# Kernel optimization log

Measured on AMD Instinct MI355X. Metric: run time of the kernel, lower is better.

The kernel has to match this reference:

```python
import jax, jax.numpy as jnp
import numpy as np

B, S, D, FD = 2, 2048, 1024, 4096
EPS_LN = 1e-5


def _l2norm(x):
    n = jnp.linalg.norm(x, axis=-1, keepdims=True)
    return x / jnp.maximum(n, 1e-12)


def _layernorm(x, w, b):
    m = x.mean(-1, keepdims=True)
    v = ((x - m) ** 2).mean(-1, keepdims=True)
    return (x - m) / jnp.sqrt(v + EPS_LN) * w + b


def _spl(x, mu_w, mu_b, gate, proto):
    # cosine-similarity gated linear (SparseProtoLinear)
    scores = _l2norm(x) @ _l2norm(proto).T          # [..., out]
    rw = jax.nn.relu(scores - gate)
    comp = x @ mu_w.T + mu_b
    return comp * rw


def _rotate_half(x):
    h = x.shape[-1] // 2
    return jnp.concatenate([-x[..., h:], x[..., :h]], axis=-1)


def _forward(x, cos, sin,
             ln1_w, ln1_b, ln2_w, ln2_b,
             qkv_mu, qkv_proto, qkv_bias, qkv_gate,
             o_mu, o_proto, o_bias, o_gate,
             f1_mu, f1_proto, f1_bias, f1_gate,
             f2_mu, f2_proto, f2_bias, f2_gate,
             pt_qkv, pt_o, pt_f1, pt_f2,
             pln_qkv_w, pln_qkv_b, pln_o_w, pln_o_b,
             pln_f1_w, pln_f1_b, pln_f2_w, pln_f2_b,
             prev_qkv, prev_o, prev_f1, prev_f2):
    # effective protos: proto_weight + LN(Linear(prev_proto))
    eff_qkv = qkv_proto + _layernorm(prev_qkv @ pt_qkv.T, pln_qkv_w, pln_qkv_b)
    eff_o   = o_proto   + _layernorm(prev_o   @ pt_o.T,   pln_o_w,   pln_o_b)
    eff_f1  = f1_proto  + _layernorm(prev_f1  @ pt_f1.T,  pln_f1_w,  pln_f1_b)
    eff_f2  = f2_proto  + _layernorm(prev_f2  @ pt_f2.T,  pln_f2_w,  pln_f2_b)

    # attention
    attn_in = _layernorm(x, ln1_w, ln1_b)
    m_qkv = _spl(attn_in, qkv_mu, qkv_bias, qkv_gate, eff_qkv)   # [B,S,3D]
    q, k, v = jnp.split(m_qkv, 3, axis=-1)
    c = cos[None]; s = sin[None]
    q = q * c + _rotate_half(q) * s
    k = k * c + _rotate_half(k) * s
    scale = 1.0 / jnp.sqrt(jnp.asarray(D, x.dtype))
    scores = jnp.einsum('bqd,bkd->bqk', q, k) * scale            # [B,S,S]
    causal = jnp.tril(jnp.ones((S, S), dtype=bool))
    scores = jnp.where(causal[None], scores, jnp.finfo(x.dtype).min)
    attn = jax.nn.softmax(scores, axis=-1)
    attn_out = jnp.einsum('bqk,bkd->bqd', attn, v)
    m_o = _spl(attn_out, o_mu, o_bias, o_gate, eff_o)
    x1 = x + m_o

    # ffn (DynamicInfiniteExpert)
    ffn_in = _layernorm(x1, ln2_w, ln2_b)
    m1 = _spl(ffn_in, f1_mu, f1_bias, f1_gate, eff_f1)           # [B,S,FD]
    h = jax.nn.relu(m1)
    m2 = _spl(h, f2_mu, f2_bias, f2_gate, eff_f2)                # [B,S,D]
    return x1 + m2


def setup_inputs() -> dict:
    key = jax.random.key(0)
    ks = iter(jax.random.split(key, 64))

    def nrm(shape, scale=1.0):
        return jax.random.normal(next(ks), shape, dtype=jnp.float32) * scale

    # RoPE tables
    pos = np.arange(S, dtype=np.float32)
    inv_freq = 1.0 / (10000.0 ** (np.arange(0, D, 2, dtype=np.float32) / D))
    freqs = np.outer(pos, inv_freq)
    emb = np.concatenate([freqs, freqs], axis=-1)
    cos = jnp.asarray(np.cos(emb)); sin = jnp.asarray(np.sin(emb))

    sD = 1.0 / np.sqrt(D); sF = 1.0 / np.sqrt(FD)
    inp = {
        'x': nrm((B, S, D)), 'cos': cos, 'sin': sin,
        'ln1_w': jnp.ones((D,)), 'ln1_b': jnp.zeros((D,)),
        'ln2_w': jnp.ones((D,)), 'ln2_b': jnp.zeros((D,)),
        'qkv_mu': nrm((3 * D, D), sD), 'qkv_proto': nrm((3 * D, D), sD),
        'qkv_bias': jnp.zeros((3 * D,)), 'qkv_gate': jnp.zeros((3 * D,)),
        'o_mu': nrm((D, D), sD), 'o_proto': nrm((D, D), sD),
        'o_bias': jnp.zeros((D,)), 'o_gate': jnp.zeros((D,)),
        'f1_mu': nrm((FD, D), sD), 'f1_proto': nrm((FD, D), sD),
        'f1_bias': jnp.zeros((FD,)), 'f1_gate': jnp.zeros((FD,)),
        'f2_mu': nrm((D, FD), sF), 'f2_proto': nrm((D, FD), sF),
        'f2_bias': jnp.zeros((D,)), 'f2_gate': jnp.zeros((D,)),
        'pt_qkv': nrm((D, D), sD), 'pt_o': nrm((D, D), sD),
        'pt_f1': nrm((D, D), sD), 'pt_f2': nrm((FD, FD), sF),
        'pln_qkv_w': jnp.ones((D,)), 'pln_qkv_b': jnp.zeros((D,)),
        'pln_o_w': jnp.ones((D,)), 'pln_o_b': jnp.zeros((D,)),
        'pln_f1_w': jnp.ones((D,)), 'pln_f1_b': jnp.zeros((D,)),
        'pln_f2_w': jnp.ones((FD,)), 'pln_f2_b': jnp.zeros((FD,)),
        'prev_qkv': nrm((3 * D, D), sD), 'prev_o': nrm((D, D), sD),
        'prev_f1': nrm((FD, D), sD), 'prev_f2': nrm((D, FD), sF),
    }
    return inp


def reference(x, cos, sin,
              ln1_w, ln1_b, ln2_w, ln2_b,
              qkv_mu, qkv_proto, qkv_bias, qkv_gate,
              o_mu, o_proto, o_bias, o_gate,
              f1_mu, f1_proto, f1_bias, f1_gate,
              f2_mu, f2_proto, f2_bias, f2_gate,
              pt_qkv, pt_o, pt_f1, pt_f2,
              pln_qkv_w, pln_qkv_b, pln_o_w, pln_o_b,
              pln_f1_w, pln_f1_b, pln_f2_w, pln_f2_b,
              prev_qkv, prev_o, prev_f1, prev_f2):
    return _forward(x, cos, sin, ln1_w, ln1_b, ln2_w, ln2_b,
                    qkv_mu, qkv_proto, qkv_bias, qkv_gate,
                    o_mu, o_proto, o_bias, o_gate,
                    f1_mu, f1_proto, f1_bias, f1_gate,
                    f2_mu, f2_proto, f2_bias, f2_gate,
                    pt_qkv, pt_o, pt_f1, pt_f2,
                    pln_qkv_w, pln_qkv_b, pln_o_w, pln_o_b,
                    pln_f1_w, pln_f1_b, pln_f2_w, pln_f2_b,
                    prev_qkv, prev_o, prev_f1, prev_f2)
```

## Files before the change

### kernel.cpp

```cpp
#include <hip/hip_runtime.h>
#include <cstdint>

typedef unsigned short u16;
typedef __attribute__((ext_vector_type(8))) short sh8;
typedef __attribute__((ext_vector_type(4))) float f32x4;

struct __align__(8) us4 { u16 x, y, z, w; };

__device__ __forceinline__ u16 f2bf(float f) {
  unsigned u = __float_as_uint(f);
  u += 0x7FFFu + ((u >> 16) & 1u);
  return (u16)(u >> 16);
}
__device__ __forceinline__ float bf2f(u16 h) {
  return __uint_as_float((unsigned)h << 16);
}
__device__ __forceinline__ float invnorm(float nrm) {
  return fminf(rsqrtf(nrm), 1e12f);
}

__device__ __forceinline__ float blk_sum(float v, float* red) {
#pragma unroll
  for (int o = 32; o; o >>= 1) v += __shfl_xor(v, o);
  __syncthreads();
  if ((threadIdx.x & 63) == 0) red[threadIdx.x >> 6] = v;
  __syncthreads();
  return red[0] + red[1] + red[2] + red[3];
}
__device__ __forceinline__ float blk_max(float v, float* red) {
#pragma unroll
  for (int o = 32; o; o >>= 1) v = fmaxf(v, __shfl_xor(v, o));
  __syncthreads();
  if ((threadIdx.x & 63) == 0) red[threadIdx.x >> 6] = v;
  __syncthreads();
  return fmaxf(fmaxf(red[0], red[1]), fmaxf(red[2], red[3]));
}

__global__ void fillv(float* __restrict__ o, long n, float v) {
  long i = (long)blockIdx.x * blockDim.x + threadIdx.x;
  if (i < n) o[i] = v;
}

struct CvtN10 {
  const float* s[10];
  u16* d[10];
  long n4[10];
};
__global__ void cvt_many(CvtN10 c) {
  int z = blockIdx.y;
  long i = (long)blockIdx.x * blockDim.x + threadIdx.x;
  if (i >= c.n4[z]) return;
  float4 v = ((const float4*)c.s[z])[i];
  us4 o; o.x = f2bf(v.x); o.y = f2bf(v.y); o.z = f2bf(v.z); o.w = f2bf(v.w);
  ((us4*)c.d[z])[i] = o;
}

#define GL16(gp, lp)                                                        \
  __builtin_amdgcn_global_load_lds(                                         \
      (const __attribute__((address_space(1))) void*)(gp),                  \
      (__attribute__((address_space(3))) void*)(lp), 16, 0, 0)

#define G256_PROLOG()                                                          \
  extern __shared__ u16 lds[];                                                 \
  int tid = threadIdx.x;                                                       \
  int wid = tid >> 6, lane = tid & 63;                                         \
  int wm = wid >> 2, wn = wid & 3;                                             \
  int bm = blockIdx.x, bn = blockIdx.y;                                        \
  int k0s = 0, nt;                                                             \
  if (kchunk) {                                                                \
    k0s = blockIdx.z * kchunk;                                                 \
    nt = kchunk >> 5;                                                          \
  } else {                                                                     \
    nt = K >> 5;                                                               \
  }                                                                            \
  const size_t baseArow = (size_t)bm * 256;                                    \
  const size_t baseBrow = (size_t)bn * 256;                                    \
  int ci = (wid << 6) + lane;                                                  \
  int rowS = ci >> 2;                                                          \
  int kcS = (ci ^ (ci >> 3)) & 3;                                              \
  const u16* gA0 = A + (baseArow + rowS) * lda + k0s + kcS * 8;                \
  const u16* gA1 = gA0 + (size_t)128 * lda;                                    \
  const u16* gB0 = B + (baseBrow + rowS) * ldb + k0s + kcS * 8;                \
  const u16* gB1 = gB0 + (size_t)128 * ldb;                                    \
  u16* dBase = lds + (wid << 9);                                               \
  int l15 = lane & 15, l4 = lane >> 4;                                         \
  int aoff[8], boff[4];                                                        \
  _Pragma("unroll") for (int fr = 0; fr < 8; ++fr) {                           \
    int by = (wm * 128 + fr * 16 + l15) * 64 + l4 * 16;                        \
    aoff[fr] = (by ^ (((by >> 7) & 3) << 4)) >> 1;                             \
  }                                                                            \
  _Pragma("unroll") for (int fc = 0; fc < 4; ++fc) {                           \
    int by = (wn * 64 + fc * 16 + l15) * 64 + l4 * 16;                         \
    boff[fc] = 8192 + ((by ^ (((by >> 7) & 3) << 4)) >> 1);                    \
  }                                                                            \
  f32x4 acc[8][4];                                                             \
  const f32x4 zf = {0.f, 0.f, 0.f, 0.f};                                       \
  _Pragma("unroll") for (int i = 0; i < 8; ++i)                                \
    _Pragma("unroll") for (int j = 0; j < 4; ++j) acc[i][j] = zf;

#define STAGE256(ts)                                                  \
  do {                                                                \
    int ss_ = (ts) & 3;                                               \
    int kk_ = (ts) << 5;                                              \
    u16* d_ = dBase + ss_ * 16384;                                    \
    GL16(gA0 + kk_, d_);                                              \
    GL16(gA1 + kk_, d_ + 4096);                                       \
    GL16(gB0 + kk_, d_ + 8192);                                       \
    GL16(gB1 + kk_, d_ + 12288);                                      \
  } while (0)

#define G256_KLOOP()                                                           \
  STAGE256(0);                                                                 \
  STAGE256(1);                                                                 \
  STAGE256(2);                                                                 \
  asm volatile("s_waitcnt vmcnt(8)" ::: "memory");                             \
  __builtin_amdgcn_s_barrier();                                                \
  __builtin_amdgcn_sched_barrier(0);                                           \
  for (int t = 0; t < nt; ++t) {                                               \
    int ts = t + 3;                                                            \
    if (ts < nt) STAGE256(ts);                                                 \
    const u16* sl = lds + (t & 3) * 16384;                                     \
    sh8 af[8], bfv[4];                                                         \
    _Pragma("unroll") for (int fc = 0; fc < 4; ++fc)                           \
        bfv[fc] = *(const sh8*)(sl + boff[fc]);                                \
    _Pragma("unroll") for (int fr = 0; fr < 8; ++fr)                           \
        af[fr] = *(const sh8*)(sl + aoff[fr]);                                 \
    __builtin_amdgcn_s_setprio(1);                                             \
    _Pragma("unroll") for (int fr = 0; fr < 8; ++fr)                           \
      _Pragma("unroll") for (int fc = 0; fc < 4; ++fc)                         \
        acc[fr][fc] = __builtin_amdgcn_mfma_f32_16x16x32_bf16(                 \
            af[fr], bfv[fc], acc[fr][fc], 0, 0, 0);                            \
    __builtin_amdgcn_s_setprio(0);                                             \
    int rem = nt - 2 - t;                                                      \
    if (rem >= 2)      asm volatile("s_waitcnt vmcnt(8)" ::: "memory");        \
    else if (rem == 1) asm volatile("s_waitcnt vmcnt(4)" ::: "memory");        \
    else if (rem == 0) asm volatile("s_waitcnt vmcnt(0)" ::: "memory");        \
    if (t < nt - 1) {                                                          \
      __builtin_amdgcn_s_barrier();                                            \
      __builtin_amdgcn_sched_barrier(0);                                       \
    }                                                                          \
  }

template <typename CT>
__global__ __launch_bounds__(512, 1) void gemm256(
    const u16* __restrict__ A, const u16* __restrict__ B, CT* __restrict__ C,
    int M, int N, int K, int lda, int ldb, int kchunk) {
  if (kchunk) C += (size_t)blockIdx.z * M * (size_t)N;
  G256_PROLOG();
  G256_KLOOP();
  int cr = l4 << 2, cc = l15;
  const size_t rbase = baseArow + wm * 128 + cr;
  const size_t cbase = baseBrow + wn * 64 + cc;
#pragma unroll
  for (int fr = 0; fr < 8; ++fr)
#pragma unroll
    for (int fc = 0; fc < 4; ++fc) {
      size_t cb = (rbase + fr * 16) * (size_t)N + cbase + fc * 16;
#pragma unroll
      for (int r = 0; r < 4; ++r) {
        float v = acc[fr][fc][r];
        if constexpr (sizeof(CT) == 2) C[cb + (size_t)r * N] = (CT)f2bf(v);
        else                           C[cb + (size_t)r * N] = v;
      }
    }
}

template <typename CT>
__global__ __launch_bounds__(256, 2) void gemm_bt(
    const u16* __restrict__ A, const u16* __restrict__ B, CT* __restrict__ C,
    int M, int N, int K, int lda, int ldb,
    int mode, long zsA, long zsB, long zsC) {
  int bm, bn;
  int z = blockIdx.z;
  if (mode == 3) {
    int t = blockIdx.x;
    int m = (int)floorf((sqrtf(8.f * t + 1.f) - 1.f) * 0.5f);
    while ((m + 1) * (m + 2) / 2 <= t) ++m;
    while (m * (m + 1) / 2 > t) --m;
    bm = m; bn = t - m * (m + 1) / 2;
  } else {
    bm = blockIdx.x; bn = blockIdx.y;
  }
  int k0s = 0, k0e = K;
  if (mode == 1) {
    int kc = K / gridDim.z;
    k0s = z * kc; k0e = k0s + kc;
    C += (size_t)z * M * (size_t)N;
  } else if (mode == 2 || mode == 3) {
    A += (size_t)z * zsA; B += (size_t)z * zsB; C += (size_t)z * zsC;
  } else if (mode == 4) {
    A += (size_t)z * zsA; B += (size_t)z * zsB; C += (size_t)z * zsC;
    k0e = (bm + 1) * 128;
  } else if (mode == 5) {
    int Mz = (int)((zsB >> (z * 16)) & 0xFFFF);
    if (bm * 128 >= Mz) return;
    A += (size_t)z * zsA; B += (size_t)z * 1048576; C += (size_t)z * zsC;
  }

  __shared__ __align__(16) u16 As[128 * 32];
  __shared__ __align__(16) u16 Bs[128 * 32];
  int tid = threadIdx.x, wid = tid >> 6, lane = tid & 63;
  int wr = (wid >> 1) << 6, wc = (wid & 1) << 6;
  int lr = lane & 15, lk = (lane >> 4) << 3;

  f32x4 acc[4][4];
  const f32x4 zf = {0.f, 0.f, 0.f, 0.f};
#pragma unroll
  for (int i = 0; i < 4; ++i)
#pragma unroll
    for (int j = 0; j < 4; ++j) acc[i][j] = zf;

  int r0 = tid >> 2, c0 = (tid & 3) << 3;
  const size_t baseA = (size_t)bm * 128, baseB = (size_t)bn * 128;
  const u16* Ab = A + baseA * lda;
  const u16* Bp = B + baseB * ldb;

  for (int k0 = k0s; k0 < k0e; k0 += 32) {
    GL16(Ab + (size_t)r0 * lda + k0 + c0, As + (wid << 9));
    GL16(Ab + (size_t)(64 + r0) * lda + k0 + c0, As + 2048 + (wid << 9));
    GL16(Bp + (size_t)r0 * ldb + k0 + c0, Bs + (wid << 9));
    GL16(Bp + (size_t)(64 + r0) * ldb + k0 + c0, Bs + 2048 + (wid << 9));
    __syncthreads();
    sh8 af[4], bfr[4];
#pragma unroll
    for (int f = 0; f < 4; ++f) {
      af[f]  = *(const sh8*)(As + (wr + f * 16 + lr) * 32 + lk);
      bfr[f] = *(const sh8*)(Bs + (wc + f * 16 + lr) * 32 + lk);
    }
#pragma unroll
    for (int i = 0; i < 4; ++i)
#pragma unroll
      for (int j = 0; j < 4; ++j)
        acc[i][j] = __builtin_amdgcn_mfma_f32_16x16x32_bf16(af[i], bfr[j], acc[i][j], 0, 0, 0);
    __syncthreads();
  }

  int cr = (lane >> 4) << 2, cc = lane & 15;
#pragma unroll
  for (int i = 0; i < 4; ++i)
#pragma unroll
    for (int j = 0; j < 4; ++j) {
      size_t cb = (baseA + wr + i * 16 + cr) * (size_t)N + (baseB + wc + j * 16 + cc);
#pragma unroll
      for (int r = 0; r < 4; ++r) {
        float v = acc[i][j][r];
        if constexpr (sizeof(CT) == 2) C[cb + (size_t)r * N] = (CT)f2bf(v);
        else                           C[cb + (size_t)r * N] = v;
      }
    }
}

__global__ void ln_rows(const float* __restrict__ X, const float* __restrict__ w,
                        const float* __restrict__ b, u16* __restrict__ Y,
                        float* __restrict__ norms, int C) {
  __shared__ float red[4];
  int row = blockIdx.x;
  const float* x = X + (size_t)row * C;
  int nv = C >> 2;
  float s = 0.f, ss = 0.f;
  for (int i = threadIdx.x; i < nv; i += 256) {
    float4 v = ((const float4*)x)[i];
    s += v.x + v.y + v.z + v.w;
    ss += v.x * v.x + v.y * v.y + v.z * v.z + v.w * v.w;
  }
  s = blk_sum(s, red);
  ss = blk_sum(ss, red);
  float mean = s / C;
  float inv = rsqrtf(fmaxf(ss / C - mean * mean, 0.f) + 1e-5f);
  float nrm = 0.f;
  for (int i = threadIdx.x; i < nv; i += 256) {
    float4 v = ((const float4*)x)[i];
    float4 wv = ((const float4*)w)[i];
    float4 bv = ((const float4*)b)[i];
    float y0 = (v.x - mean) * inv * wv.x + bv.x;
    float y1 = (v.y - mean) * inv * wv.y + bv.y;
    float y2 = (v.z - mean) * inv * wv.z + bv.z;
    float y3 = (v.w - mean) * inv * wv.w + bv.w;
    nrm += y0 * y0 + y1 * y1 + y2 * y2 + y3 * y3;
    us4 o; o.x = f2bf(y0); o.y = f2bf(y1); o.z = f2bf(y2); o.w = f2bf(y3);
    ((us4*)(Y + (size_t)row * C))[i] = o;
  }
  nrm = blk_sum(nrm, red);
  if (threadIdx.x == 0) norms[row] = invnorm(nrm);
}

__global__ void ln_add_norm(const u16* __restrict__ T0, const u16* __restrict__ T1,
                            const float* __restrict__ P,
                            const float* __restrict__ w, const float* __restrict__ b,
                            u16* __restrict__ E, float* __restrict__ norms, int C) {
  __shared__ float red[4];
  int row = blockIdx.x;
  const us4* t0 = (const us4*)(T0 + (size_t)row * C);
  const us4* t1 = T1 ? (const us4*)(T1 + (size_t)row * C) : nullptr;
  const float* p = P + (size_t)row * C;
  int nv = C >> 2;
  float s = 0.f, ss = 0.f;
  for (int i = threadIdx.x; i < nv; i += 256) {
    us4 v = t0[i];
    float f0 = bf2f(v.x), f1 = bf2f(v.y), f2 = bf2f(v.z), f3 = bf2f(v.w);
    if (t1) {
      us4 v1 = t1[i];
      f0 += bf2f(v1.x); f1 += bf2f(v1.y); f2 += bf2f(v1.z); f3 += bf2f(v1.w);
    }
    s += f0 + f1 + f2 + f3;
    ss += f0 * f0 + f1 * f1 + f2 * f2 + f3 * f3;
  }
  s = blk_sum(s, red);
  ss = blk_sum(ss, red);
  float mean = s / C;
  float inv = rsqrtf(fmaxf(ss / C - mean * mean, 0.f) + 1e-5f);
  float nrm = 0.f;
  for (int i = threadIdx.x; i < nv; i += 256) {
    us4 v = t0[i];
    float f0 = bf2f(v.x), f1 = bf2f(v.y), f2 = bf2f(v.z), f3 = bf2f(v.w);
    if (t1) {
      us4 v1 = t1[i];
      f0 += bf2f(v1.x); f1 += bf2f(v1.y); f2 += bf2f(v1.z); f3 += bf2f(v1.w);
    }
    float4 pv = ((const float4*)p)[i];
    float4 wv = ((const float4*)w)[i];
    float4 bv = ((const float4*)b)[i];
    float y0 = pv.x + (f0 - mean) * inv * wv.x + bv.x;
    float y1 = pv.y + (f1 - mean) * inv * wv.y + bv.y;
    float y2 = pv.z + (f2 - mean) * inv * wv.z + bv.z;
    float y3 = pv.w + (f3 - mean) * inv * wv.w + bv.w;
    nrm += y0 * y0 + y1 * y1 + y2 * y2 + y3 * y3;
    us4 o; o.x = f2bf(y0); o.y = f2bf(y1); o.z = f2bf(y2); o.w = f2bf(y3);
    *(us4*)(E + (size_t)row * C + (i << 2)) = o;
  }
  nrm = blk_sum(nrm, red);
  if (threadIdx.x == 0) norms[row] = invnorm(nrm);
}

struct Lan3 {
  const u16* T[3];
  const float* P[3]; const float* w[3]; const float* b[3];
  u16* E[3]; float* nr[3]; int M[3];
};
__global__ void lan_many(Lan3 L) {
  __shared__ float red[4];
  int z = blockIdx.y;
  int row = blockIdx.x;
  if (row >= L.M[z]) return;
  int i = threadIdx.x;
  us4 v = ((const us4*)(L.T[z] + (size_t)row * 1024))[i];
  float f0 = bf2f(v.x), f1 = bf2f(v.y), f2 = bf2f(v.z), f3 = bf2f(v.w);
  float s = blk_sum(f0 + f1 + f2 + f3, red);
  float ss = blk_sum(f0 * f0 + f1 * f1 + f2 * f2 + f3 * f3, red);
  float mean = s * (1.f / 1024.f);
  float inv = rsqrtf(fmaxf(ss * (1.f / 1024.f) - mean * mean, 0.f) + 1e-5f);
  float4 pv = ((const float4*)(L.P[z] + (size_t)row * 1024))[i];
  float4 wv = ((const float4*)L.w[z])[i];
  float4 bv = ((const float4*)L.b[z])[i];
  float y0 = pv.x + (f0 - mean) * inv * wv.x + bv.x;
  float y1 = pv.y + (f1 - mean) * inv * wv.y + bv.y;
  float y2 = pv.z + (f2 - mean) * inv * wv.z + bv.z;
  float y3 = pv.w + (f3 - mean) * inv * wv.w + bv.w;
  us4 o; o.x = f2bf(y0); o.y = f2bf(y1); o.z = f2bf(y2); o.w = f2bf(y3);
  ((us4*)(L.E[z] + (size_t)row * 1024))[i] = o;
  float nrm = blk_sum(y0 * y0 + y1 * y1 + y2 * y2 + y3 * y3, red);
  if (threadIdx.x == 0) L.nr[z][row] = invnorm(nrm);
}

__global__ void rownorm_bf(const u16* __restrict__ X, float* __restrict__ norms, int C) {
  __shared__ float red[4];
  int row = blockIdx.x;
  const us4* x = (const us4*)(X + (size_t)row * C);
  int nv = C >> 2;
  float nrm = 0.f;
  for (int i = threadIdx.x; i < nv; i += 256) {
    us4 v = x[i];
    float a = bf2f(v.x), b = bf2f(v.y), c = bf2f(v.z), d = bf2f(v.w);
    nrm += a * a + b * b + c * c + d * d;
  }
  nrm = blk_sum(nrm, red);
  if (threadIdx.x == 0) norms[row] = invnorm(nrm);
}

__device__ __forceinline__ void epi4(const u16* gr, int C, int c, float rr,
                                     const float* bias, const float* gate,
                                     const float* cn, float* o) {
  us4 cv = *(const us4*)(gr + c);
  us4 dv = *(const us4*)(gr + C + c);
  float4 bv = *(const float4*)(bias + c);
  float4 gv = *(const float4*)(gate + c);
  float4 nv = *(const float4*)(cn + c);
  float cf[4] = {bf2f(cv.x), bf2f(cv.y), bf2f(cv.z), bf2f(cv.w)};
  float df[4] = {bf2f(dv.x), bf2f(dv.y), bf2f(dv.z), bf2f(dv.w)};
  float bb[4] = {bv.x, bv.y, bv.z, bv.w};
  float gg[4] = {gv.x, gv.y, gv.z, gv.w};
  float nn[4] = {nv.x, nv.y, nv.z, nv.w};
#pragma unroll
  for (int j = 0; j < 4; ++j) {
    float sc = df[j] * (rr * nn[j]);
    o[j] = (cf[j] + bb[j]) * fmaxf(sc - gg[j], 0.f);
  }
}

__global__ void spl_rope_row(const u16* __restrict__ G, const float* __restrict__ bias,
                             const float* __restrict__ gate, const float* __restrict__ rn,
                             const float* __restrict__ cn, const float* __restrict__ CT_,
                             const float* __restrict__ ST_, u16* __restrict__ MQ) {
  int r = blockIdx.x;
  int s = r & 2047;
  const u16* gr = G + (size_t)r * 6144;
  u16* outr = MQ + (size_t)r * 3072;
  float rr = rn[r];
  int t = threadIdx.x;

  int qk = (t >> 7);
  int c = qk * 1024 + ((t & 127) << 2);
  int d = c - qk * 1024;
  float a0[4], a1[4];
  epi4(gr, 3072, c, rr, bias, gate, cn, a0);
  epi4(gr, 3072, c + 512, rr, bias, gate, cn, a1);
  const float* ct = CT_ + (size_t)s * 1024;
  const float* st = ST_ + (size_t)s * 1024;
  float4 c0 = *(const float4*)(ct + d);
  float4 s0 = *(const float4*)(st + d);
  float4 c1 = *(const float4*)(ct + d + 512);
  float4 s1 = *(const float4*)(st + d + 512);
  float cc0[4] = {c0.x, c0.y, c0.z, c0.w}, ss0[4] = {s0.x, s0.y, s0.z, s0.w};
  float cc1[4] = {c1.x, c1.y, c1.z, c1.w}, ss1[4] = {s1.x, s1.y, s1.z, s1.w};
  us4 o0, o1;
  o0.x = f2bf(a0[0] * cc0[0] - a1[0] * ss0[0]);
  o0.y = f2bf(a0[1] * cc0[1] - a1[1] * ss0[1]);
  o0.z = f2bf(a0[2] * cc0[2] - a1[2] * ss0[2]);
  o0.w = f2bf(a0[3] * cc0[3] - a1[3] * ss0[3]);
  o1.x = f2bf(a1[0] * cc1[0] + a0[0] * ss1[0]);
  o1.y = f2bf(a1[1] * cc1[1] + a0[1] * ss1[1]);
  o1.z = f2bf(a1[2] * cc1[2] + a0[2] * ss1[2]);
  o1.w = f2bf(a1[3] * cc1[3] + a0[3] * ss1[3]);
  *(us4*)(outr + c) = o0;
  *(us4*)(outr + c + 512) = o1;

  int cv_ = 2048 + (t << 2);
  float vv[4];
  epi4(gr, 3072, cv_, rr, bias, gate, cn, vv);
  us4 ov; ov.x = f2bf(vv[0]); ov.y = f2bf(vv[1]); ov.z = f2bf(vv[2]); ov.w = f2bf(vv[3]);
  *(us4*)(outr + cv_) = ov;
}

__global__ void spl_f1_row(const u16* __restrict__ G, const float* __restrict__ bias,
                           const float* __restrict__ gate, const float* __restrict__ rn,
                           const float* __restrict__ cn, u16* __restrict__ H,
                           float* __restrict__ rn_h) {
  __shared__ float red[4];
  int r = blockIdx.x;
  const u16* gr = G + (size_t)r * 8192;
  u16* hr = H + (size_t)r * 4096;
  float rr = rn[r];
  float nrm = 0.f;
  for (int c = threadIdx.x << 2; c < 4096; c += 1024) {
    float o[4];
    epi4(gr, 4096, c, rr, bias, gate, cn, o);
#pragma unroll
    for (int j = 0; j < 4; ++j) {
      o[j] = fmaxf(o[j], 0.f);
      nrm += o[j] * o[j];
    }
    us4 ov; ov.x = f2bf(o[0]); ov.y = f2bf(o[1]); ov.z = f2bf(o[2]); ov.w = f2bf(o[3]);
    *(us4*)(hr + c) = ov;
  }
  nrm = blk_sum(nrm, red);
  if (threadIdx.x == 0) rn_h[r] = invnorm(nrm);
}

__global__ void spl_o_ln_row(const u16* __restrict__ G, const float* __restrict__ bias,
                             const float* __restrict__ gate, const float* __restrict__ rn,
                             const float* __restrict__ cn, const float* __restrict__ xres,
                             const float* __restrict__ lw, const float* __restrict__ lb,
                             float* __restrict__ X1, u16* __restrict__ Y,
                             float* __restrict__ rn_ffn) {
  __shared__ float red[4];
  int r = blockIdx.x;
  int c = threadIdx.x << 2;
  const u16* gr = G + (size_t)r * 2048;
  float o[4];
  epi4(gr, 1024, c, rn[r], bias, gate, cn, o);
  float4 rv = *(const float4*)(xres + (size_t)r * 1024 + c);
  o[0] += rv.x; o[1] += rv.y; o[2] += rv.z; o[3] += rv.w;
  float4 xo = {o[0], o[1], o[2], o[3]};
  *(float4*)(X1 + (size_t)r * 1024 + c) = xo;
  float s = o[0] + o[1] + o[2] + o[3];
  float ss = o[0] * o[0] + o[1] * o[1] + o[2] * o[2] + o[3] * o[3];
  s = blk_sum(s, red);
  ss = blk_sum(ss, red);
  float mean = s * (1.f / 1024.f);
  float inv = rsqrtf(fmaxf(ss * (1.f / 1024.f) - mean * mean, 0.f) + 1e-5f);
  float4 wv = *(const float4*)(lw + c);
  float4 bv = *(const float4*)(lb + c);
  float ww[4] = {wv.x, wv.y, wv.z, wv.w}, bb[4] = {bv.x, bv.y, bv.z, bv.w};
  float nrm = 0.f;
  us4 ov;
  u16* op = (u16*)&ov;
#pragma unroll
  for (int j = 0; j < 4; ++j) {
    float y = (o[j] - mean) * inv * ww[j] + bb[j];
    nrm += y * y;
    op[j] = f2bf(y);
  }
  *(us4*)(Y + (size_t)r * 1024 + c) = ov;
  nrm = blk_sum(nrm, red);
  if (threadIdx.x == 0) rn_ffn[r] = invnorm(nrm);
}

__global__ void spl_epi_p(const u16* __restrict__ G0, const u16* __restrict__ G1,
                          const float* __restrict__ bias, const float* __restrict__ gate,
                          const float* __restrict__ rn, const float* __restrict__ cn,
                          const float* __restrict__ resid, float* __restrict__ out) {
  int r = blockIdx.x;
  int c = threadIdx.x << 2;
  size_t rowb = (size_t)r * 2048;
  us4 c0 = *(const us4*)(G0 + rowb + c);
  us4 c1 = *(const us4*)(G1 + rowb + c);
  us4 d0 = *(const us4*)(G0 + rowb + 1024 + c);
  us4 d1 = *(const us4*)(G1 + rowb + 1024 + c);
  float4 bv = *(const float4*)(bias + c);
  float4 gv = *(const float4*)(gate + c);
  float4 nv = *(const float4*)(cn + c);
  float4 rv = *(const float4*)(resid + (size_t)r * 1024 + c);
  float rr = rn[r];
  float cf[4] = {bf2f(c0.x) + bf2f(c1.x), bf2f(c0.y) + bf2f(c1.y),
                 bf2f(c0.z) + bf2f(c1.z), bf2f(c0.w) + bf2f(c1.w)};
  float df[4] = {bf2f(d0.x) + bf2f(d1.x), bf2f(d0.y) + bf2f(d1.y),
                 bf2f(d0.z) + bf2f(d1.z), bf2f(d0.w) + bf2f(d1.w)};
  float bb[4] = {bv.x, bv.y, bv.z, bv.w};
  float gg[4] = {gv.x, gv.y, gv.z, gv.w};
  float nn[4] = {nv.x, nv.y, nv.z, nv.w};
  float re[4] = {rv.x, rv.y, rv.z, rv.w};
  float4 ov;
  float* op = (float*)&ov;
#pragma unroll
  for (int j = 0; j < 4; ++j) {
    float sc = df[j] * (rr * nn[j]);
    op[j] = (cf[j] + bb[j]) * fmaxf(sc - gg[j], 0.f) + re[j];
  }
  *(float4*)(out + (size_t)r * 1024 + c) = ov;
}

__global__ void vtrans(const u16* __restrict__ MQ, u16* __restrict__ VT) {
  __shared__ u16 tile[32][33];
  int b = blockIdx.z;
  int s0 = blockIdx.x << 5, d0 = blockIdx.y << 5;
  int tx = threadIdx.x, ty = threadIdx.y;
  for (int r = ty; r < 32; r += 8)
    tile[r][tx] = MQ[((size_t)(b * 2048 + s0 + r)) * 3072 + 2048 + d0 + tx];
  __syncthreads();
  for (int r = ty; r < 32; r += 8)
    VT[(size_t)b * 1024 * 2048 + (size_t)(d0 + r) * 2048 + s0 + tx] = tile[tx][r];
}

__global__ void softmax_causal(const float* __restrict__ S, u16* __restrict__ P) {
  __shared__ float red[4];
  int b = blockIdx.x >> 11;
  int q = blockIdx.x & 2047;
  const float* row = S + ((size_t)b << 22) + (size_t)q * 2048;
  u16* prow = P + ((size_t)b << 22) + (size_t)q * 2048;
  int nv = q + 1;
  int wcap = ((q >> 7) + 1) << 7;
  int base = threadIdx.x * 8;
  float e[8];
  float m = -3.4e38f;
  float xv[8];
  bool live = base < nv;
  if (live) {
    float4 a = *(const float4*)(row + base);
    float4 bq = *(const float4*)(row + base + 4);
    xv[0] = a.x; xv[1] = a.y; xv[2] = a.z; xv[3] = a.w;
    xv[4] = bq.x; xv[5] = bq.y; xv[6] = bq.z; xv[7] = bq.w;
#pragma unroll
    for (int j = 0; j < 8; ++j) {
      xv[j] *= 0.03125f;
      if (base + j < nv) m = fmaxf(m, xv[j]);
    }
  }
  m = blk_max(m, red);
  float ssum = 0.f;
#pragma unroll
  for (int j = 0; j < 8; ++j) {
    e[j] = (live && base + j < nv) ? __expf(xv[j] - m) : 0.f;
    ssum += e[j];
  }
  ssum = blk_sum(ssum, red);
  float invs = 1.f / ssum;
  if (base < wcap) {
    us4 o;
    o.x = f2bf(e[0] * invs); o.y = f2bf(e[1] * invs);
    o.z = f2bf(e[2] * invs); o.w = f2bf(e[3] * invs);
    ((us4*)prow)[threadIdx.x * 2] = o;
    o.x = f2bf(e[4] * invs); o.y = f2bf(e[5] * invs);
    o.z = f2bf(e[6] * invs); o.w = f2bf(e[7] * invs);
    ((us4*)prow)[threadIdx.x * 2 + 1] = o;
  }
}

extern "C" void kernel_launch(void* const* d_in, const int* in_sizes, int n_in,
                              void* d_out, int out_size, void* d_ws, size_t ws_size,
                              hipStream_t stream) {
  (void)in_sizes;
  const float* x         = (const float*)d_in[0];
  const float* cosT      = (const float*)d_in[1];
  const float* sinT      = (const float*)d_in[2];
  const float* ln1_w     = (const float*)d_in[3];
  const float* ln1_b     = (const float*)d_in[4];
  const float* ln2_w     = (const float*)d_in[5];
  const float* ln2_b     = (const float*)d_in[6];
  const float* qkv_mu    = (const float*)d_in[7];
  const float* qkv_proto = (const float*)d_in[8];
  const float* qkv_bias  = (const float*)d_in[9];
  const float* qkv_gate  = (const float*)d_in[10];
  const float* o_mu      = (const float*)d_in[11];
  const float* o_proto   = (const float*)d_in[12];
  const float* o_bias    = (const float*)d_in[13];
  const float* o_gate    = (const float*)d_in[14];
  const float* f1_mu     = (const float*)d_in[15];
  const float* f1_proto  = (const float*)d_in[16];
  const float* f1_bias   = (const float*)d_in[17];
  const float* f1_gate   = (const float*)d_in[18];
  const float* f2_mu     = (const float*)d_in[19];
  const float* f2_proto  = (const float*)d_in[20];
  const float* f2_bias   = (const float*)d_in[21];
  const float* f2_gate   = (const float*)d_in[22];
  const float* pt_qkv    = (const float*)d_in[23];
  const float* pt_o      = (const float*)d_in[24];
  const float* pt_f1     = (const float*)d_in[25];
  const float* pt_f2     = (const float*)d_in[26];
  const float* pln_qkv_w = (const float*)d_in[27];
  const float* pln_qkv_b = (const float*)d_in[28];
  const float* pln_o_w   = (const float*)d_in[29];
  const float* pln_o_b   = (const float*)d_in[30];
  const float* pln_f1_w  = (const float*)d_in[31];
  const float* pln_f1_b  = (const float*)d_in[32];
  const float* pln_f2_w  = (const float*)d_in[33];
  const float* pln_f2_b  = (const float*)d_in[34];
  const float* prev_qkv  = (const float*)d_in[35];
  const float* prev_o    = (const float*)d_in[36];
  const float* prev_f1   = (const float*)d_in[37];
  const float* prev_f2   = (const float*)d_in[38];

  const long D = 1024, TD = 3072, FD = 4096, R = 4096;

  char* W = (char*)d_ws;
  size_t off = 0;
  auto alloc = [&](size_t bytes) {
    void* p = W + off;
    off = (off + bytes + 255) & ~(size_t)255;
    return p;
  };
  char* GOUT = (char*)alloc(67108864);
  u16*  RC   = (u16*)alloc(33554432);
  u16*  wq   = (u16*)alloc(2 * TD * D * 2);
  u16*  wo   = (u16*)alloc(2 * D * D * 2);
  u16*  wf1  = (u16*)alloc(2 * FD * D * 2);
  u16*  wf2  = (u16*)alloc(2 * D * FD * 2);
  float* X1  = (float*)alloc(R * D * 4);
  u16*  P1   = (u16*)alloc(R * D * 2);
  u16*  VT   = (u16*)alloc(2 * D * 2048 * 2);
  u16*  AOB  = (u16*)alloc(R * D * 2);
  float* pnq     = (float*)alloc(TD * 4);
  float* pno     = (float*)alloc(D * 4);
  float* pnf1    = (float*)alloc(FD * 4);
  float* pnf2    = (float*)alloc(D * 4);
  float* rn_ain  = (float*)alloc(R * 4);
  float* rn_aout = (float*)alloc(R * 4);
  float* rn_ffn  = (float*)alloc(R * 4);
  float* rn_h    = (float*)alloc(R * 4);
  size_t need = off;

  if (n_in < 39 || need > ws_size) {
    long n = out_size;
    fillv<<<dim3((unsigned)((n + 255) / 256)), 256, 0, stream>>>((float*)d_out, n, 12345.0f);
    return;
  }

  u16* SA = (u16*)GOUT;
  u16* SB = (u16*)(GOUT + 25165824);
  float* SCORES = (float*)GOUT;
  u16* PB = (u16*)(GOUT + 33554432);

  {
    CvtN10 c;
    c.s[0] = prev_f1;  c.d[0] = SA;            c.n4[0] = (FD * D) >> 2;
    c.s[1] = prev_qkv; c.d[1] = SA + 4194304;  c.n4[1] = (TD * D) >> 2;
    c.s[2] = prev_o;   c.d[2] = SA + 8388608;  c.n4[2] = (D * D) >> 2;
    c.s[3] = pt_f1;    c.d[3] = SB;            c.n4[3] = (D * D) >> 2;
    c.s[4] = pt_qkv;   c.d[4] = SB + 1048576;  c.n4[4] = (D * D) >> 2;
    c.s[5] = pt_o;     c.d[5] = SB + 2097152;  c.n4[5] = (D * D) >> 2;
    c.s[6] = qkv_mu;   c.d[6] = wq;            c.n4[6] = (TD * D) >> 2;
    c.s[7] = f1_mu;    c.d[7] = wf1;           c.n4[7] = (FD * D) >> 2;
    c.s[8] = o_mu;     c.d[8] = wo;            c.n4[8] = (D * D) >> 2;
    c.s[9] = f2_mu;    c.d[9] = wf2;           c.n4[9] = (D * FD) >> 2;
    cvt_many<<<dim3(4096, 10), 256, 0, stream>>>(c);
  }
  {
    long Mz = 4096L | (3072L << 16) | (1024L << 32);
    gemm_bt<u16><<<dim3(32, 8, 3), 256, 0, stream>>>(
        SA, SB, RC, 4096, 1024, 1024, 1024, 1024, 5, 4194304, Mz, 4194304);
  }
  {
    Lan3 L;
    L.T[0] = RC;           L.P[0] = f1_proto;  L.w[0] = pln_f1_w;  L.b[0] = pln_f1_b;
    L.E[0] = wf1 + (size_t)FD * D;  L.nr[0] = pnf1;  L.M[0] = 4096;
    L.T[1] = RC + 4194304; L.P[1] = qkv_proto; L.w[1] = pln_qkv_w; L.b[1] = pln_qkv_b;
    L.E[1] = wq + (size_t)TD * D;   L.nr[1] = pnq;   L.M[1] = 3072;
    L.T[2] = RC + 8388608; L.P[2] = o_proto;   L.w[2] = pln_o_w;   L.b[2] = pln_o_b;
    L.E[2] = wo + (size_t)D * D;    L.nr[2] = pno;   L.M[2] = 1024;
    lan_many<<<dim3(4096, 3), 256, 0, stream>>>(L);
  }
  {
    CvtN10 c = {};
    c.s[0] = prev_f2; c.d[0] = SA; c.n4[0] = (D * FD) >> 2;
    c.s[1] = pt_f2;   c.d[1] = SB; c.n4[1] = ((long)FD * FD) >> 2;
    cvt_many<<<dim3(16384, 2), 256, 0, stream>>>(c);
  }
  gemm_bt<u16><<<dim3(8, 32, 2), 256, 0, stream>>>(
      SA, SB, RC, 1024, 4096, 4096, 4096, 4096, 1, 0, 0, 0);
  ln_add_norm<<<1024, 256, 0, stream>>>(RC, RC + 4194304, f2_proto, pln_f2_w, pln_f2_b,
                                        wf2 + (size_t)D * FD, pnf2, 4096);

  ln_rows<<<4096, 256, 0, stream>>>(x, ln1_w, ln1_b, P1, rn_ain, 1024);
  gemm256<u16><<<dim3(16, 24), 512, 131072, stream>>>(
      P1, wq, (u16*)GOUT, 4096, 6144, 1024, 1024, 1024, 0);
  spl_rope_row<<<4096, 256, 0, stream>>>(
      (u16*)GOUT, qkv_bias, qkv_gate, rn_ain, pnq, cosT, sinT, RC);

  vtrans<<<dim3(64, 32, 2), dim3(32, 8), 0, stream>>>(RC, VT);
  gemm_bt<float><<<dim3(136, 1, 2), 256, 0, stream>>>(
      RC, RC + 1024, SCORES, 2048, 2048, 1024, 3072, 3072,
      3, 2048L * 3072, 2048L * 3072, 1L << 22);
  softmax_causal<<<4096, 256, 0, stream>>>(SCORES, PB);
  gemm_bt<u16><<<dim3(16, 8, 2), 256, 0, stream>>>(
      PB, VT, AOB, 2048, 1024, 2048, 2048, 2048,
      4, 1L << 22, 1024L * 2048, 2048L * 1024);
  rownorm_bf<<<4096, 256, 0, stream>>>(AOB, rn_aout, 1024);

  gemm_bt<u16><<<dim3(32, 16, 1), 256, 0, stream>>>(
      AOB, wo, (u16*)GOUT, 4096, 2048, 1024, 1024, 1024, 0, 0, 0, 0);
  spl_o_ln_row<<<4096, 256, 0, stream>>>(
      (u16*)GOUT, o_bias, o_gate, rn_aout, pno, x, ln2_w, ln2_b, X1, P1, rn_ffn);

  gemm256<u16><<<dim3(16, 32), 512, 131072, stream>>>(
      P1, wf1, (u16*)GOUT, 4096, 8192, 1024, 1024, 1024, 0);
  spl_f1_row<<<4096, 256, 0, stream>>>(
      (u16*)GOUT, f1_bias, f1_gate, rn_ffn, pnf1, RC, rn_h);
  gemm256<u16><<<dim3(16, 8, 2), 512, 131072, stream>>>(
      RC, wf2, (u16*)GOUT, 4096, 2048, 4096, 4096, 4096, 2048);
  spl_epi_p<<<4096, 256, 0, stream>>>(
      (u16*)GOUT, (u16*)GOUT + 8388608, f2_bias, f2_gate, rn_h, pnf2,
      X1, (float*)d_out);
}
```

Before: 558.3 us.

## Add XCD-aware block swizzle, store attention scores in bf16, retile QKV GEMM

Adds an XCD-aware remapping of workgroup indices in both GEMM kernels so that neighbouring tiles land on the same chiplet and share L2. The QK^T scores are now written as bf16 instead of fp32, which halves score-matrix traffic into the softmax. The QKV projection also moves from the 256-tile gemm256 kernel to the 128-tile gemm_bt kernel. Rounding scores to bf16 before the softmax loses some precision, and the smaller tiles for QKV may lower data reuse.

```diff
diff --git a/kernel.cpp b/kernel.cpp
--- a/kernel.cpp
+++ b/kernel.cpp
@@ -17,6 +17,11 @@
 }
 __device__ __forceinline__ float invnorm(float nrm) {
   return fminf(rsqrtf(nrm), 1e12f);
+}
+__device__ __forceinline__ int xcd_swz(int flat, int nwg) {
+  if (nwg & 7) return flat;
+  int q = nwg >> 3;
+  return (flat & 7) * q + (flat >> 3);
 }
 
 __device__ __forceinline__ float blk_sum(float v, float* red) {
@@ -65,7 +70,9 @@
   int tid = threadIdx.x;                                                       \
   int wid = tid >> 6, lane = tid & 63;                                         \
   int wm = wid >> 2, wn = wid & 3;                                             \
-  int bm = blockIdx.x, bn = blockIdx.y;                                        \
+  int flatb = xcd_swz(blockIdx.x + blockIdx.y * gridDim.x,                     \
+                      gridDim.x * gridDim.y);                                  \
+  int bm = flatb % gridDim.x, bn = flatb / gridDim.x;                          \
   int k0s = 0, nt;                                                             \
   if (kchunk) {                                                                \
     k0s = blockIdx.z * kchunk;                                                 \
@@ -173,13 +180,15 @@
   int bm, bn;
   int z = blockIdx.z;
   if (mode == 3) {
-    int t = blockIdx.x;
+    int t = xcd_swz(blockIdx.x, gridDim.x);
     int m = (int)floorf((sqrtf(8.f * t + 1.f) - 1.f) * 0.5f);
     while ((m + 1) * (m + 2) / 2 <= t) ++m;
     while (m * (m + 1) / 2 > t) --m;
     bm = m; bn = t - m * (m + 1) / 2;
   } else {
-    bm = blockIdx.x; bn = blockIdx.y;
+    int flatb = xcd_swz(blockIdx.x + blockIdx.y * gridDim.x,
+                        gridDim.x * gridDim.y);
+    bm = flatb % gridDim.x; bn = flatb / gridDim.x;
   }
   int k0s = 0, k0e = K;
   if (mode == 1) {
@@ -551,11 +560,11 @@
     VT[(size_t)b * 1024 * 2048 + (size_t)(d0 + r) * 2048 + s0 + tx] = tile[tx][r];
 }
 
-__global__ void softmax_causal(const float* __restrict__ S, u16* __restrict__ P) {
+__global__ void softmax_causal(const u16* __restrict__ S, u16* __restrict__ P) {
   __shared__ float red[4];
   int b = blockIdx.x >> 11;
   int q = blockIdx.x & 2047;
-  const float* row = S + ((size_t)b << 22) + (size_t)q * 2048;
+  const u16* row = S + ((size_t)b << 22) + (size_t)q * 2048;
   u16* prow = P + ((size_t)b << 22) + (size_t)q * 2048;
   int nv = q + 1;
   int wcap = ((q >> 7) + 1) << 7;
@@ -565,10 +574,10 @@
   float xv[8];
   bool live = base < nv;
   if (live) {
-    float4 a = *(const float4*)(row + base);
-    float4 bq = *(const float4*)(row + base + 4);
-    xv[0] = a.x; xv[1] = a.y; xv[2] = a.z; xv[3] = a.w;
-    xv[4] = bq.x; xv[5] = bq.y; xv[6] = bq.z; xv[7] = bq.w;
+    us4 a = *(const us4*)(row + base);
+    us4 bq = *(const us4*)(row + base + 4);
+    xv[0] = bf2f(a.x); xv[1] = bf2f(a.y); xv[2] = bf2f(a.z); xv[3] = bf2f(a.w);
+    xv[4] = bf2f(bq.x); xv[5] = bf2f(bq.y); xv[6] = bf2f(bq.z); xv[7] = bf2f(bq.w);
 #pragma unroll
     for (int j = 0; j < 8; ++j) {
       xv[j] *= 0.03125f;
@@ -676,8 +685,8 @@
 
   u16* SA = (u16*)GOUT;
   u16* SB = (u16*)(GOUT + 25165824);
-  float* SCORES = (float*)GOUT;
-  u16* PB = (u16*)(GOUT + 33554432);
+  u16* SCORESB = (u16*)GOUT;
+  u16* PB = (u16*)(GOUT + 16777216);
 
   {
     CvtN10 c;
@@ -720,16 +729,16 @@
                                         wf2 + (size_t)D * FD, pnf2, 4096);
 
   ln_rows<<<4096, 256, 0, stream>>>(x, ln1_w, ln1_b, P1, rn_ain, 1024);
-  gemm256<u16><<<dim3(16, 24), 512, 131072, stream>>>(
-      P1, wq, (u16*)GOUT, 4096, 6144, 1024, 1024, 1024, 0);
+  gemm_bt<u16><<<dim3(32, 48, 1), 256, 0, stream>>>(
+      P1, wq, (u16*)GOUT, 4096, 6144, 1024, 1024, 1024, 0, 0, 0, 0);
   spl_rope_row<<<4096, 256, 0, stream>>>(
       (u16*)GOUT, qkv_bias, qkv_gate, rn_ain, pnq, cosT, sinT, RC);
 
   vtrans<<<dim3(64, 32, 2), dim3(32, 8), 0, stream>>>(RC, VT);
-  gemm_bt<float><<<dim3(136, 1, 2), 256, 0, stream>>>(
-      RC, RC + 1024, SCORES, 2048, 2048, 1024, 3072, 3072,
+  gemm_bt<u16><<<dim3(136, 1, 2), 256, 0, stream>>>(
+      RC, RC + 1024, SCORESB, 2048, 2048, 1024, 3072, 3072,
       3, 2048L * 3072, 2048L * 3072, 1L << 22);
-  softmax_causal<<<4096, 256, 0, stream>>>(SCORES, PB);
+  softmax_causal<<<4096, 256, 0, stream>>>(SCORESB, PB);
   gemm_bt<u16><<<dim3(16, 8, 2), 256, 0, stream>>>(
       PB, VT, AOB, 2048, 1024, 2048, 2048, 2048,
       4, 1L << 22, 1024L * 2048, 2048L * 1024);
```

Result: slower. 583.6 us (+4.5%).
